# Kernel tuning notes

Measured on AMD Instinct MI355X. Metric: run time of the kernel, lower is better.

## Reference

```python
import jax, jax.numpy as jnp
import numpy as np

N_NODES = 50000
N_EDGES = 800000
D_FEAT = 64
D_HID = 64
N_CLASSES = 16


def gcn_conv(x, row, col, ew, W, b, n_nodes):
    """PyG GCNConv (normalize=True, add_self_loops=True) with edge weights.
    out[c] = sum_{(r,c) in E+selfloops} d^-1/2[r] * w * d^-1/2[c] * (x @ W)[r] + b
    """
    h = x @ W  # [N, out]
    loop = jnp.arange(n_nodes)
    row = jnp.concatenate([row, loop])
    col = jnp.concatenate([col, loop])
    w = jnp.concatenate([ew, jnp.ones((n_nodes,), dtype=ew.dtype)])
    deg = jax.ops.segment_sum(w, col, num_segments=n_nodes)  # in-degree (weighted)
    dinv = jnp.where(deg > 0, jax.lax.rsqrt(deg), 0.0)
    norm = dinv[row] * w * dinv[col]  # [E+N]
    msgs = norm[:, None] * h[row]  # [E+N, out]
    out = jax.ops.segment_sum(msgs, col, num_segments=n_nodes)
    return out + b


def setup_inputs() -> dict:
    key = jax.random.key(0)
    ks = jax.random.split(key, 12)
    x = jax.random.normal(ks[0], (N_NODES, D_FEAT), dtype=jnp.float32)
    edge_index = jax.random.randint(ks[1], (2, N_EDGES), 0, N_NODES, dtype=jnp.int64)
    edge_attr = jax.random.uniform(ks[2], (N_EDGES,), dtype=jnp.float32)
    s1 = 1.0 / np.sqrt(D_FEAT)
    s2 = 1.0 / np.sqrt(D_HID)
    W1 = jax.random.uniform(ks[3], (D_FEAT, D_HID), minval=-s1, maxval=s1, dtype=jnp.float32)
    b1 = jnp.zeros((D_HID,), dtype=jnp.float32)
    W2 = jax.random.uniform(ks[4], (D_HID, D_HID), minval=-s2, maxval=s2, dtype=jnp.float32)
    b2 = jnp.zeros((D_HID,), dtype=jnp.float32)
    Wm1 = jax.random.uniform(ks[5], (D_HID, D_HID), minval=-s2, maxval=s2, dtype=jnp.float32)
    bm1 = jax.random.uniform(ks[6], (D_HID,), minval=-s2, maxval=s2, dtype=jnp.float32)
    Wm2 = jax.random.uniform(ks[7], (D_HID, N_CLASSES), minval=-s2, maxval=s2, dtype=jnp.float32)
    bm2 = jax.random.uniform(ks[8], (N_CLASSES,), minval=-s2, maxval=s2, dtype=jnp.float32)
    return {"x": x, "edge_index": edge_index, "edge_attr": edge_attr,
            "W1": W1, "b1": b1, "W2": W2, "b2": b2,
            "Wm1": Wm1, "bm1": bm1, "Wm2": Wm2, "bm2": bm2}


def reference(x, edge_index, edge_attr, W1, b1, W2, b2, Wm1, bm1, Wm2, bm2):
    # eval-mode forward: dropout is identity
    n = x.shape[0]
    row, col = edge_index[0], edge_index[1]
    h = jax.nn.relu(gcn_conv(x, row, col, edge_attr, W1, b1, n))
    h = jax.nn.relu(gcn_conv(h, row, col, edge_attr, W2, b2, n))
    h = jax.nn.relu(h @ Wm1 + bm1)
    logits = h @ Wm2 + bm2
    return jax.nn.sigmoid(logits)
```

## Files before the change

kernel.cpp:

```cpp
#include <hip/hip_runtime.h>
#include <hip/hip_fp16.h>
#include <math.h>

#define D 64
#define CAP 48
#define PSZ 256
#define NBIN 196
#define BCAP 4864
#define TSTRIDE 16
#define FILLB 512
#define ITMAX 7
#define EWINV (1.0f / 65535.0f)
#define GNODES 16
#define ROWU4 (CAP / 4)
#define STU4  (GNODES * ROWU4)

typedef unsigned long long u64;
typedef unsigned uint4v __attribute__((ext_vector_type(4)));


__global__ void __launch_bounds__(256, 2) k_mm1_fill(
        const float* __restrict__ X, const float* __restrict__ W1,
        __half* __restrict__ Y, int n, int mmBlocks,
        const int* __restrict__ row, const int* __restrict__ col,
        const float* __restrict__ ew, int* __restrict__ tails,
        u64* __restrict__ binsG, int E) {
    __shared__ int hist[NBIN], startS[NBIN], curS[NBIN], baseS[NBIN];
    __shared__ int gsum[16];

    if (blockIdx.x < mmBlocks) {
        int lane = threadIdx.x & 63;
        float wreg[64];
#pragma unroll
        for (int k = 0; k < 64; ++k) wreg[k] = W1[k * 64 + lane];
        int wv  = blockIdx.x * 4 + (threadIdx.x >> 6);
        int nwv = mmBlocks * 4;
        const float4* x4 = (const float4*)X;
        for (int r = wv; r < n; r += nwv) {
            float acc = 0.f;
#pragma unroll
            for (int j = 0; j < 16; ++j) {
                float4 v = x4[r * 16 + j];
                acc += v.x * wreg[4 * j + 0] + v.y * wreg[4 * j + 1]
                     + v.z * wreg[4 * j + 2] + v.w * wreg[4 * j + 3];
            }
            Y[r * 64 + lane] = __float2half(acc);
        }
    } else {
        int fb  = blockIdx.x - mmBlocks;
        int tid = threadIdx.x;
        int chunk = (E + FILLB - 1) / FILLB;
        int e0 = fb * chunk;
        int e1 = min(e0 + chunk, E);

        for (int i = tid; i < NBIN; i += 256) hist[i] = 0;
        __syncthreads();

        unsigned lov[ITMAX], ewv[ITMAX];
        unsigned char binv[ITMAX];
#pragma unroll
        for (int it = 0; it < ITMAX; ++it) {
            int e = e0 + it * 256 + tid;
            if (e < e1) {
                int c = col[e];
                int bn = c >> 8;
                binv[it] = (unsigned char)bn;
                lov[it]  = ((unsigned)row[e] << 8) | (unsigned)(c & (PSZ - 1));
                ewv[it]  = __float_as_uint(ew[e]);
                atomicAdd(&hist[bn], 1);
            }
        }
        __syncthreads();
        if (tid < 13) {
            int s = 0, hi = min(tid * 16 + 16, NBIN);
            for (int i = tid * 16; i < hi; ++i) s += hist[i];
            gsum[tid] = s;
        }
        __syncthreads();
        if (tid < NBIN) {
            int s = 0, g = tid >> 4;
            for (int i = 0; i < g; ++i) s += gsum[i];
            for (int i = g << 4; i < tid; ++i) s += hist[i];
            startS[tid] = s;
            curS[tid]   = s;
            baseS[tid]  = atomicAdd(&tails[tid * TSTRIDE], hist[tid]);
        }
        __syncthreads();
#pragma unroll
        for (int it = 0; it < ITMAX; ++it) {
            int e = e0 + it * 256 + tid;
            if (e < e1) {
                int bn = binv[it];
                int p  = atomicAdd(&curS[bn], 1);
                int dst = baseS[bn] + (p - startS[bn]);
                if (dst < BCAP)
                    binsG[(size_t)bn * BCAP + dst] = ((u64)ewv[it] << 32) | lov[it];
            }
        }
    }
}


__global__ void k_binscatter(const u64* __restrict__ binsG,
                             const int* __restrict__ tails,
                             int* __restrict__ cnt, float* __restrict__ dinv,
                             unsigned* __restrict__ bucket, __half* __restrict__ xw1, int n) {
    __shared__ int   lc[PSZ];
    __shared__ float lsum[PSZ];
    int bin = blockIdx.x, tid = threadIdx.x;
    for (int i = tid; i < PSZ; i += blockDim.x) { lc[i] = 0; lsum[i] = 0.f; }
    __syncthreads();
    int m = tails[bin * TSTRIDE];
    if (m > BCAP) m = BCAP;
    const u64* src = binsG + (size_t)bin * BCAP;
    int base = bin * PSZ;
    for (int i = tid; i < m; i += blockDim.x) {
        u64 v = __builtin_nontemporal_load(&src[i]);
        unsigned lo = (unsigned)v;
        int cOff = lo & (PSZ - 1);
        unsigned r = (lo >> 8) & 0xFFFF;
        float wv = __uint_as_float((unsigned)(v >> 32));
        float qf = rintf(wv * 65535.0f);
        int p = atomicAdd(&lc[cOff], 1);
        atomicAdd(&lsum[cOff], qf);
        if (p < CAP)
            bucket[(size_t)(base + cOff) * CAP + p] = ((unsigned)qf << 16) | r;
    }
    __syncthreads();
    for (int i = tid; i < PSZ; i += blockDim.x) {
        int node = base + i;
        if (node < n) {
            cnt[node] = lc[i];
            float dv = rsqrtf(1.0f + lsum[i] * EWINV);
            dinv[node] = dv;
            lsum[i] = dv;
        }
    }
    __syncthreads();
    int lim = min(PSZ, n - base);
    float4* x4 = (float4*)(xw1 + (size_t)base * 64);
    for (int idx = tid; idx < lim * 8; idx += blockDim.x) {
        float dv = lsum[idx >> 3];
        float4 raw = x4[idx];
        __half2* h = (__half2*)&raw;
#pragma unroll
        for (int j = 0; j < 4; ++j) {
            float lo = __half2float(__low2half(h[j]))  * dv;
            float hi = __half2float(__high2half(h[j])) * dv;
            h[j] = __halves2half2(__float2half(lo), __float2half(hi));
        }
        x4[idx] = raw;
    }
}


__device__ __forceinline__ float gather_lds(const __half* __restrict__ xw,
                                            const unsigned* ep, int c,
                                            float dd, float bb, int node, int lane) {
    float self = __half2float(xw[node * 64 + lane]);
    float a0 = 0.f, a1 = 0.f, a2 = 0.f, a3 = 0.f;
    int j = 0;
    for (; j + 8 <= c; j += 8) {
        unsigned e0 = ep[j + 0], e1 = ep[j + 1], e2 = ep[j + 2], e3 = ep[j + 3];
        unsigned e4 = ep[j + 4], e5 = ep[j + 5], e6 = ep[j + 6], e7 = ep[j + 7];
        float v0 = __half2float(xw[(e0 & 0xFFFFu) * 64 + lane]);
        float v1 = __half2float(xw[(e1 & 0xFFFFu) * 64 + lane]);
        float v2 = __half2float(xw[(e2 & 0xFFFFu) * 64 + lane]);
        float v3 = __half2float(xw[(e3 & 0xFFFFu) * 64 + lane]);
        float v4 = __half2float(xw[(e4 & 0xFFFFu) * 64 + lane]);
        float v5 = __half2float(xw[(e5 & 0xFFFFu) * 64 + lane]);
        float v6 = __half2float(xw[(e6 & 0xFFFFu) * 64 + lane]);
        float v7 = __half2float(xw[(e7 & 0xFFFFu) * 64 + lane]);
        a0 += (float)(e0 >> 16) * v0;  a1 += (float)(e1 >> 16) * v1;
        a2 += (float)(e2 >> 16) * v2;  a3 += (float)(e3 >> 16) * v3;
        a0 += (float)(e4 >> 16) * v4;  a1 += (float)(e5 >> 16) * v5;
        a2 += (float)(e6 >> 16) * v6;  a3 += (float)(e7 >> 16) * v7;
    }
    for (; j + 4 <= c; j += 4) {
        unsigned e0 = ep[j + 0], e1 = ep[j + 1], e2 = ep[j + 2], e3 = ep[j + 3];
        a0 += (float)(e0 >> 16) * __half2float(xw[(e0 & 0xFFFFu) * 64 + lane]);
        a1 += (float)(e1 >> 16) * __half2float(xw[(e1 & 0xFFFFu) * 64 + lane]);
        a2 += (float)(e2 >> 16) * __half2float(xw[(e2 & 0xFFFFu) * 64 + lane]);
        a3 += (float)(e3 >> 16) * __half2float(xw[(e3 & 0xFFFFu) * 64 + lane]);
    }
    for (; j < c; ++j) {
        unsigned e0 = ep[j];
        a0 += (float)(e0 >> 16) * __half2float(xw[(e0 & 0xFFFFu) * 64 + lane]);
    }
    return dd * (self + EWINV * ((a0 + a1) + (a2 + a3))) + bb;
}


__global__ void __launch_bounds__(256) k_gather_mm(
        const __half* __restrict__ xw, const float* __restrict__ dinv,
        const float* __restrict__ b, const int* __restrict__ cnt,
        const unsigned* __restrict__ bucket, const float* __restrict__ W,
        __half* __restrict__ out, int n) {
    __shared__ float ws[64][64];
    __shared__ float hs[4][64];
    __shared__ unsigned ebuf[2][GNODES][CAP];
    __shared__ int   cbuf[2][GNODES];
    __shared__ float dbuf[2][GNODES];
    int tid = threadIdx.x, lane = tid & 63, w = tid >> 6;
    for (int i = tid; i < 4096; i += 256) ws[i >> 6][i & 63] = W[i];
    float bb = b[lane];

    int ngg = (n + GNODES - 1) / GNODES;
    int gg = blockIdx.x;
    if (gg < ngg) {
        int base = gg * GNODES;
        int lim = min(GNODES, n - base);
        if (tid < lim * ROWU4)
            ((uint4v*)&ebuf[0][0][0])[tid] =
                __builtin_nontemporal_load((const uint4v*)(bucket + (size_t)base * CAP) + tid);
        if (tid >= STU4 && tid - STU4 < lim)        cbuf[0][tid - STU4] = cnt[base + tid - STU4];
        if (tid >= STU4 + 16 && tid - STU4 - 16 < lim) dbuf[0][tid - STU4 - 16] = dinv[base + tid - STU4 - 16];
    }
    __syncthreads();
    int cur = 0;
    while (gg < ngg) {
        int ggN = gg + gridDim.x;
        bool haveN = (ggN < ngg);
        uint4v nE = (uint4v)(0u); int nC = 0; float nD = 0.f; int limN = 0;
        if (haveN) {
            int baseN = ggN * GNODES;
            limN = min(GNODES, n - baseN);
            if (tid < limN * ROWU4)
                nE = __builtin_nontemporal_load((const uint4v*)(bucket + (size_t)baseN * CAP) + tid);
            if (tid >= STU4 && tid - STU4 < limN)        nC = cnt[baseN + tid - STU4];
            if (tid >= STU4 + 16 && tid - STU4 - 16 < limN) nD = dinv[baseN + tid - STU4 - 16];
        }
        int base = gg * GNODES;
#pragma unroll
        for (int q = 0; q < 4; ++q) {
            int ln = w * 4 + q;
            int node = base + ln;
            if (node < n) {
                float dd = dbuf[cur][ln];
                int c = cbuf[cur][ln]; if (c > CAP) c = CAP;
                float h = fmaxf(gather_lds(xw, &ebuf[cur][ln][0], c, dd, bb, node, lane), 0.0f);
                hs[w][lane] = h;
                __builtin_amdgcn_wave_barrier();
                float s = 0.f;
#pragma unroll
                for (int k = 0; k < 64; ++k) s += hs[w][k] * ws[k][lane];
                __builtin_amdgcn_wave_barrier();
                out[node * 64 + lane] = __float2half(dd * s);
            }
        }
        if (!haveN) break;
        __syncthreads();
        if (tid < limN * ROWU4) ((uint4v*)&ebuf[cur ^ 1][0][0])[tid] = nE;
        if (tid >= STU4 && tid - STU4 < limN)        cbuf[cur ^ 1][tid - STU4] = nC;
        if (tid >= STU4 + 16 && tid - STU4 - 16 < limN) dbuf[cur ^ 1][tid - STU4 - 16] = nD;
        __syncthreads();
        gg = ggN; cur ^= 1;
    }
}


__global__ void __launch_bounds__(256) k_gather_head(
        const __half* __restrict__ xw, const float* __restrict__ dinv,
        const float* __restrict__ b, const int* __restrict__ cnt,
        const unsigned* __restrict__ bucket,
        const float* __restrict__ Wm1, const float* __restrict__ bm1,
        const float* __restrict__ Wm2, const float* __restrict__ bm2,
        float* __restrict__ out, int n) {
    __shared__ __half w1h[64][64];
    __shared__ float w2[64][16];
    __shared__ float sb1[64];
    __shared__ float sb2[16];
    __shared__ float h2s[4][64];
    __shared__ float h3s[4][64];
    __shared__ unsigned ebuf[2][GNODES][CAP];
    __shared__ int   cbuf[2][GNODES];
    __shared__ float dbuf[2][GNODES];
    int tid = threadIdx.x, lane = tid & 63, w = tid >> 6;
    for (int i = tid; i < 4096; i += 256) w1h[i >> 6][i & 63] = __float2half(Wm1[i]);
    for (int i = tid; i < 1024; i += 256) w2[i >> 4][i & 15] = Wm2[i];
    if (tid < 64) sb1[tid] = bm1[tid];
    if (tid < 16) sb2[tid] = bm2[tid];
    float bb = b[lane];

    int ngg = (n + GNODES - 1) / GNODES;
    int gg = blockIdx.x;
    if (gg < ngg) {
        int base = gg * GNODES;
        int lim = min(GNODES, n - base);
        if (tid < lim * ROWU4)
            ((uint4v*)&ebuf[0][0][0])[tid] =
                __builtin_nontemporal_load((const uint4v*)(bucket + (size_t)base * CAP) + tid);
        if (tid >= STU4 && tid - STU4 < lim)        cbuf[0][tid - STU4] = cnt[base + tid - STU4];
        if (tid >= STU4 + 16 && tid - STU4 - 16 < lim) dbuf[0][tid - STU4 - 16] = dinv[base + tid - STU4 - 16];
    }
    __syncthreads();
    int cur = 0;
    while (gg < ngg) {
        int ggN = gg + gridDim.x;
        bool haveN = (ggN < ngg);
        uint4v nE = (uint4v)(0u); int nC = 0; float nD = 0.f; int limN = 0;
        if (haveN) {
            int baseN = ggN * GNODES;
            limN = min(GNODES, n - baseN);
            if (tid < limN * ROWU4)
                nE = __builtin_nontemporal_load((const uint4v*)(bucket + (size_t)baseN * CAP) + tid);
            if (tid >= STU4 && tid - STU4 < limN)        nC = cnt[baseN + tid - STU4];
            if (tid >= STU4 + 16 && tid - STU4 - 16 < limN) nD = dinv[baseN + tid - STU4 - 16];
        }
        int base = gg * GNODES;
#pragma unroll
        for (int q = 0; q < 4; ++q) {
            int ln = w * 4 + q;
            int node = base + ln;
            if (node < n) {
                float dd = dbuf[cur][ln];
                int c = cbuf[cur][ln]; if (c > CAP) c = CAP;
                float h2 = fmaxf(gather_lds(xw, &ebuf[cur][ln][0], c, dd, bb, node, lane), 0.0f);
                h2s[w][lane] = h2;
                __builtin_amdgcn_wave_barrier();
                float s = sb1[lane];
#pragma unroll
                for (int k = 0; k < 64; ++k) s += h2s[w][k] * __half2float(w1h[k][lane]);
                h3s[w][lane] = fmaxf(s, 0.0f);
                __builtin_amdgcn_wave_barrier();
                if (lane < 16) {
                    float s2 = sb2[lane];
#pragma unroll
                    for (int k = 0; k < 64; ++k) s2 += h3s[w][k] * w2[k][lane];
                    out[node * 16 + lane] = 1.0f / (1.0f + expf(-s2));
                }
                __builtin_amdgcn_wave_barrier();
            }
        }
        if (!haveN) break;
        __syncthreads();
        if (tid < limN * ROWU4) ((uint4v*)&ebuf[cur ^ 1][0][0])[tid] = nE;
        if (tid >= STU4 && tid - STU4 < limN)        cbuf[cur ^ 1][tid - STU4] = nC;
        if (tid >= STU4 + 16 && tid - STU4 - 16 < limN) dbuf[cur ^ 1][tid - STU4 - 16] = nD;
        __syncthreads();
        gg = ggN; cur ^= 1;
    }
}


extern "C" void kernel_launch(void* const* d_in, const int* in_sizes, int n_in,
                              void* d_out, int out_size, void* d_ws, size_t ws_size,
                              hipStream_t stream) {
    const float* x   = (const float*)d_in[0];
    const int*   ei  = (const int*)d_in[1];
    const float* ew  = (const float*)d_in[2];
    const float* W1  = (const float*)d_in[3];
    const float* b1  = (const float*)d_in[4];
    const float* W2  = (const float*)d_in[5];
    const float* b2  = (const float*)d_in[6];
    const float* Wm1 = (const float*)d_in[7];
    const float* bm1 = (const float*)d_in[8];
    const float* Wm2 = (const float*)d_in[9];
    const float* bm2 = (const float*)d_in[10];

    int n = in_sizes[0] / D;
    int E = in_sizes[1] / 2;
    const int* row = ei;
    const int* col = ei + E;

    char* wsb = (char*)d_ws;
    unsigned* bucket = (unsigned*)wsb;
    __half* xw1    = (__half*)(bucket + (size_t)n * CAP);
    u64*    binsG  = (u64*)(xw1 + (size_t)n * D);
    __half* xw2    = (__half*)binsG;
    int*    cnt    = (int*)(binsG + (size_t)NBIN * BCAP);
    float*  dinv   = (float*)(cnt + n);
    int*    tails  = (int*)(dinv + n);
    float*  outp   = (float*)d_out;

    int mmBlocks = 1024;

    (void)hipMemsetAsync(tails, 0, (size_t)NBIN * TSTRIDE * sizeof(int), stream);
    k_mm1_fill<<<mmBlocks + FILLB, 256, 0, stream>>>(x, W1, xw1, n, mmBlocks,
                                                     row, col, ew, tails, binsG, E);
    k_binscatter<<<NBIN, 512, 0, stream>>>(binsG, tails, cnt, dinv, bucket, xw1, n);
    k_gather_mm<<<1536, 256, 0, stream>>>(xw1, dinv, b1, cnt, bucket, W2, xw2, n);
    k_gather_head<<<1536, 256, 0, stream>>>(xw2, dinv, b2, cnt, bucket,
                                            Wm1, bm1, Wm2, bm2, outp, n);
}
```

Baseline: 227.1 us.

## Process two nodes per wavefront with half2 gathers and zero-padded buckets

Result: faster. 211.2 us (-7.0%).

```diff
diff --git a/kernel.cpp b/kernel.cpp
--- a/kernel.cpp
+++ b/kernel.cpp
@@ -154,40 +154,44 @@
 }
 
 
-__device__ __forceinline__ float gather_lds(const __half* __restrict__ xw,
-                                            const unsigned* ep, int c,
-                                            float dd, float bb, int node, int lane) {
-    float self = __half2float(xw[node * 64 + lane]);
-    float a0 = 0.f, a1 = 0.f, a2 = 0.f, a3 = 0.f;
-    int j = 0;
-    for (; j + 8 <= c; j += 8) {
-        unsigned e0 = ep[j + 0], e1 = ep[j + 1], e2 = ep[j + 2], e3 = ep[j + 3];
-        unsigned e4 = ep[j + 4], e5 = ep[j + 5], e6 = ep[j + 6], e7 = ep[j + 7];
-        float v0 = __half2float(xw[(e0 & 0xFFFFu) * 64 + lane]);
-        float v1 = __half2float(xw[(e1 & 0xFFFFu) * 64 + lane]);
-        float v2 = __half2float(xw[(e2 & 0xFFFFu) * 64 + lane]);
-        float v3 = __half2float(xw[(e3 & 0xFFFFu) * 64 + lane]);
-        float v4 = __half2float(xw[(e4 & 0xFFFFu) * 64 + lane]);
-        float v5 = __half2float(xw[(e5 & 0xFFFFu) * 64 + lane]);
-        float v6 = __half2float(xw[(e6 & 0xFFFFu) * 64 + lane]);
-        float v7 = __half2float(xw[(e7 & 0xFFFFu) * 64 + lane]);
-        a0 += (float)(e0 >> 16) * v0;  a1 += (float)(e1 >> 16) * v1;
-        a2 += (float)(e2 >> 16) * v2;  a3 += (float)(e3 >> 16) * v3;
-        a0 += (float)(e4 >> 16) * v4;  a1 += (float)(e5 >> 16) * v5;
-        a2 += (float)(e6 >> 16) * v6;  a3 += (float)(e7 >> 16) * v7;
-    }
-    for (; j + 4 <= c; j += 4) {
-        unsigned e0 = ep[j + 0], e1 = ep[j + 1], e2 = ep[j + 2], e3 = ep[j + 3];
-        a0 += (float)(e0 >> 16) * __half2float(xw[(e0 & 0xFFFFu) * 64 + lane]);
-        a1 += (float)(e1 >> 16) * __half2float(xw[(e1 & 0xFFFFu) * 64 + lane]);
-        a2 += (float)(e2 >> 16) * __half2float(xw[(e2 & 0xFFFFu) * 64 + lane]);
-        a3 += (float)(e3 >> 16) * __half2float(xw[(e3 & 0xFFFFu) * 64 + lane]);
-    }
-    for (; j < c; ++j) {
-        unsigned e0 = ep[j];
-        a0 += (float)(e0 >> 16) * __half2float(xw[(e0 & 0xFFFFu) * 64 + lane]);
-    }
-    return dd * (self + EWINV * ((a0 + a1) + (a2 + a3))) + bb;
+__device__ __forceinline__ void gather_pair(const __half* __restrict__ xw,
+                                            const unsigned* ep, int cm8, int li,
+                                            float dd, float bbx, float bby,
+                                            int myNode, float& r0, float& r1) {
+    const unsigned* xwu = (const unsigned*)xw;
+    unsigned su = xwu[(size_t)myNode * 32 + li];
+    __half2 sh = *(__half2*)&su;
+    float s0 = __half2float(__low2half(sh));
+    float s1 = __half2float(__high2half(sh));
+    float a0 = 0.f, a1 = 0.f, b0 = 0.f, b1 = 0.f;
+    for (int j = 0; j < cm8; j += 8) {
+        unsigned q0 = ep[j + 0], q1 = ep[j + 1], q2 = ep[j + 2], q3 = ep[j + 3];
+        unsigned q4 = ep[j + 4], q5 = ep[j + 5], q6 = ep[j + 6], q7 = ep[j + 7];
+        unsigned u0 = xwu[(size_t)(q0 & 0xFFFFu) * 32 + li];
+        unsigned u1 = xwu[(size_t)(q1 & 0xFFFFu) * 32 + li];
+        unsigned u2 = xwu[(size_t)(q2 & 0xFFFFu) * 32 + li];
+        unsigned u3 = xwu[(size_t)(q3 & 0xFFFFu) * 32 + li];
+        unsigned u4 = xwu[(size_t)(q4 & 0xFFFFu) * 32 + li];
+        unsigned u5 = xwu[(size_t)(q5 & 0xFFFFu) * 32 + li];
+        unsigned u6 = xwu[(size_t)(q6 & 0xFFFFu) * 32 + li];
+        unsigned u7 = xwu[(size_t)(q7 & 0xFFFFu) * 32 + li];
+        __half2 h0 = *(__half2*)&u0, h1 = *(__half2*)&u1, h2 = *(__half2*)&u2, h3 = *(__half2*)&u3;
+        __half2 h4 = *(__half2*)&u4, h5 = *(__half2*)&u5, h6 = *(__half2*)&u6, h7 = *(__half2*)&u7;
+        float w0 = (float)(q0 >> 16), w1 = (float)(q1 >> 16);
+        float w2 = (float)(q2 >> 16), w3 = (float)(q3 >> 16);
+        float w4 = (float)(q4 >> 16), w5 = (float)(q5 >> 16);
+        float w6 = (float)(q6 >> 16), w7 = (float)(q7 >> 16);
+        a0 += w0 * __half2float(__low2half(h0));  a1 += w0 * __half2float(__high2half(h0));
+        b0 += w1 * __half2float(__low2half(h1));  b1 += w1 * __half2float(__high2half(h1));
+        a0 += w2 * __half2float(__low2half(h2));  a1 += w2 * __half2float(__high2half(h2));
+        b0 += w3 * __half2float(__low2half(h3));  b1 += w3 * __half2float(__high2half(h3));
+        a0 += w4 * __half2float(__low2half(h4));  a1 += w4 * __half2float(__high2half(h4));
+        b0 += w5 * __half2float(__low2half(h5));  b1 += w5 * __half2float(__high2half(h5));
+        a0 += w6 * __half2float(__low2half(h6));  a1 += w6 * __half2float(__high2half(h6));
+        b0 += w7 * __half2float(__low2half(h7));  b1 += w7 * __half2float(__high2half(h7));
+    }
+    r0 = dd * (s0 + EWINV * (a0 + b0)) + bbx;
+    r1 = dd * (s1 + EWINV * (a1 + b1)) + bby;
 }
 
 
@@ -197,13 +201,14 @@
         const unsigned* __restrict__ bucket, const float* __restrict__ W,
         __half* __restrict__ out, int n) {
     __shared__ float ws[64][64];
-    __shared__ float hs[4][64];
+    __shared__ float hs[4][2][64];
     __shared__ unsigned ebuf[2][GNODES][CAP];
     __shared__ int   cbuf[2][GNODES];
     __shared__ float dbuf[2][GNODES];
     int tid = threadIdx.x, lane = tid & 63, w = tid >> 6;
+    int hi = lane >> 5, li = lane & 31;
     for (int i = tid; i < 4096; i += 256) ws[i >> 6][i & 63] = W[i];
-    float bb = b[lane];
+    float2 bbv = ((const float2*)b)[li];
 
     int ngg = (n + GNODES - 1) / GNODES;
     int gg = blockIdx.x;
@@ -232,20 +237,29 @@
         }
         int base = gg * GNODES;
 #pragma unroll
-        for (int q = 0; q < 4; ++q) {
-            int ln = w * 4 + q;
-            int node = base + ln;
-            if (node < n) {
-                float dd = dbuf[cur][ln];
-                int c = cbuf[cur][ln]; if (c > CAP) c = CAP;
-                float h = fmaxf(gather_lds(xw, &ebuf[cur][ln][0], c, dd, bb, node, lane), 0.0f);
-                hs[w][lane] = h;
+        for (int p = 0; p < 2; ++p) {
+            int ln0 = w * 4 + p * 2;
+            int myLn = ln0 + hi;
+            int myNode = base + myLn;
+            if (myNode < n) {
+                int cA = cbuf[cur][ln0];     if (cA > CAP) cA = CAP;
+                int cB = cbuf[cur][ln0 + 1]; if (cB > CAP) cB = CAP;
+                int cm8 = (max(cA, cB) + 7) & ~7;
+                float dd = dbuf[cur][myLn];
+                float r0, r1;
+                gather_pair(xw, &ebuf[cur][myLn][0], cm8, li, dd, bbv.x, bbv.y, myNode, r0, r1);
+                *(float2*)&hs[w][hi][2 * li] = make_float2(fmaxf(r0, 0.f), fmaxf(r1, 0.f));
                 __builtin_amdgcn_wave_barrier();
-                float s = 0.f;
-#pragma unroll
-                for (int k = 0; k < 64; ++k) s += hs[w][k] * ws[k][lane];
+                float s0 = 0.f, s1 = 0.f;
+#pragma unroll
+                for (int k = 0; k < 64; ++k) {
+                    float hk = hs[w][hi][k];
+                    float2 wk = *(const float2*)&ws[k][2 * li];
+                    s0 += hk * wk.x;  s1 += hk * wk.y;
+                }
                 __builtin_amdgcn_wave_barrier();
-                out[node * 64 + lane] = __float2half(dd * s);
+                __half2 oh = __halves2half2(__float2half(dd * s0), __float2half(dd * s1));
+                ((unsigned*)out)[(size_t)myNode * 32 + li] = *(unsigned*)&oh;
             }
         }
         if (!haveN) break;
@@ -268,19 +282,19 @@
         float* __restrict__ out, int n) {
     __shared__ __half w1h[64][64];
     __shared__ float w2[64][16];
-    __shared__ float sb1[64];
     __shared__ float sb2[16];
-    __shared__ float h2s[4][64];
-    __shared__ float h3s[4][64];
+    __shared__ float h2s[4][2][64];
+    __shared__ float h3s[4][2][64];
     __shared__ unsigned ebuf[2][GNODES][CAP];
     __shared__ int   cbuf[2][GNODES];
     __shared__ float dbuf[2][GNODES];
     int tid = threadIdx.x, lane = tid & 63, w = tid >> 6;
+    int hi = lane >> 5, li = lane & 31;
     for (int i = tid; i < 4096; i += 256) w1h[i >> 6][i & 63] = __float2half(Wm1[i]);
     for (int i = tid; i < 1024; i += 256) w2[i >> 4][i & 15] = Wm2[i];
-    if (tid < 64) sb1[tid] = bm1[tid];
     if (tid < 16) sb2[tid] = bm2[tid];
-    float bb = b[lane];
+    float2 bbv  = ((const float2*)b)[li];
+    float2 bb1v = ((const float2*)bm1)[li];
 
     int ngg = (n + GNODES - 1) / GNODES;
     int gg = blockIdx.x;
@@ -309,25 +323,35 @@
         }
         int base = gg * GNODES;
 #pragma unroll
-        for (int q = 0; q < 4; ++q) {
-            int ln = w * 4 + q;
-            int node = base + ln;
-            if (node < n) {
-                float dd = dbuf[cur][ln];
-                int c = cbuf[cur][ln]; if (c > CAP) c = CAP;
-                float h2 = fmaxf(gather_lds(xw, &ebuf[cur][ln][0], c, dd, bb, node, lane), 0.0f);
-                h2s[w][lane] = h2;
+        for (int p = 0; p < 2; ++p) {
+            int ln0 = w * 4 + p * 2;
+            int myLn = ln0 + hi;
+            int myNode = base + myLn;
+            if (myNode < n) {
+                int cA = cbuf[cur][ln0];     if (cA > CAP) cA = CAP;
+                int cB = cbuf[cur][ln0 + 1]; if (cB > CAP) cB = CAP;
+                int cm8 = (max(cA, cB) + 7) & ~7;
+                float dd = dbuf[cur][myLn];
+                float r0, r1;
+                gather_pair(xw, &ebuf[cur][myLn][0], cm8, li, dd, bbv.x, bbv.y, myNode, r0, r1);
+                *(float2*)&h2s[w][hi][2 * li] = make_float2(fmaxf(r0, 0.f), fmaxf(r1, 0.f));
                 __builtin_amdgcn_wave_barrier();
-                float s = sb1[lane];
-#pragma unroll
-                for (int k = 0; k < 64; ++k) s += h2s[w][k] * __half2float(w1h[k][lane]);
-                h3s[w][lane] = fmaxf(s, 0.0f);
+                float s0 = bb1v.x, s1 = bb1v.y;
+#pragma unroll
+                for (int k = 0; k < 64; ++k) {
+                    float hk = h2s[w][hi][k];
+                    unsigned wu = *(const unsigned*)&w1h[k][2 * li];
+                    __half2 wh = *(__half2*)&wu;
+                    s0 += hk * __half2float(__low2half(wh));
+                    s1 += hk * __half2float(__high2half(wh));
+                }
+                *(float2*)&h3s[w][hi][2 * li] = make_float2(fmaxf(s0, 0.f), fmaxf(s1, 0.f));
                 __builtin_amdgcn_wave_barrier();
-                if (lane < 16) {
-                    float s2 = sb2[lane];
-#pragma unroll
-                    for (int k = 0; k < 64; ++k) s2 += h3s[w][k] * w2[k][lane];
-                    out[node * 16 + lane] = 1.0f / (1.0f + expf(-s2));
+                if (li < 16) {
+                    float s2 = sb2[li];
+#pragma unroll
+                    for (int k = 0; k < 64; ++k) s2 += h3s[w][hi][k] * w2[k][li];
+                    out[(size_t)myNode * 16 + li] = 1.0f / (1.0f + expf(-s2));
                 }
                 __builtin_amdgcn_wave_barrier();
             }
@@ -376,6 +400,7 @@
     int mmBlocks = 1024;
 
     (void)hipMemsetAsync(tails, 0, (size_t)NBIN * TSTRIDE * sizeof(int), stream);
+    (void)hipMemsetAsync(bucket, 0, (size_t)n * CAP * sizeof(unsigned), stream);
     k_mm1_fill<<<mmBlocks + FILLB, 256, 0, stream>>>(x, W1, xw1, n, mmBlocks,
                                                      row, col, ew, tails, binsG, E);
     k_binscatter<<<NBIN, 512, 0, stream>>>(binsG, tails, cnt, dinv, bucket, xw1, n);
```
